# Performance work log

Hardware: AMD Instinct MI355X
Metric: run time of the kernel (lower is better)

Reference implementation:

```python
import jax, jax.numpy as jnp
import numpy as np


def _overlap_add_fft_conv(signal, kernel):
    """Vectorized overlap-add FFT convolution.

    signal: (B, K, T) float; kernel: (B, K, R) float.
    Returns (B, K, T), identical math to the torch per-block loop (the
    ortho-normed rfft/irfft pair on the signal cancels, kernel rfft uses
    default backward norm, exactly as in the original code).
    """
    B, K, T = signal.shape
    R = kernel.shape[-1]
    fft_len = 2 << (R - 1).bit_length()          # e.g. R=4000 -> 8192
    step = fft_len - R + 1                        # hop between blocks
    pad_len = (-T) % step                         # pad T up to multiple of step
    L = T + pad_len
    n_blocks = L // step

    # split padded signal into non-overlapping blocks, zero-pad each to fft_len
    sig = jnp.pad(signal, ((0, 0), (0, 0), (0, pad_len)))
    blocks = sig.reshape(B, K, n_blocks, step)
    blocks = jnp.pad(blocks, ((0, 0), (0, 0), (0, 0), (0, fft_len - step)))

    kernel_fft = jnp.fft.rfft(
        jnp.pad(kernel, ((0, 0), (0, 0), (0, fft_len - R))))      # (B,K,F)
    block_fft = jnp.fft.rfft(blocks, norm='ortho')                # (B,K,n_blocks,F)
    conv = jnp.fft.irfft(block_fft * kernel_fft[:, :, None, :],
                         norm='ortho')                            # (B,K,n_blocks,fft_len)

    # overlap-add: block i contributes at offset i*step, length fft_len
    idx = jnp.arange(n_blocks)[:, None] * step + jnp.arange(fft_len)[None, :]
    out = jnp.zeros((B, K, L + R - 1), dtype=conv.dtype)
    out = out.at[:, :, idx].add(conv)
    return out[:, :, :T]


def setup_inputs() -> dict:
    key = jax.random.key(0)
    k1, k2 = jax.random.split(key)
    onsets = jax.random.normal(k1, (8, 8, 262144), dtype=jnp.float32)
    sources = jax.random.normal(k2, (8, 8, 4000), dtype=jnp.float32)
    return {"onsets": onsets, "sources": sources, "delay_compensation": 0}


def reference(onsets, sources, delay_compensation):
    # delay_compensation is unused in the original module as well
    return _overlap_add_fft_conv(onsets, sources)
```

## Files before the change

kernel.cpp:

```cpp
#include <hip/hip_runtime.h>

#define T_LEN 262144
#define R_LEN 4000
#define NCH 64
#define WIN 12288
#define NCHUNK 126
#define V_OFF 4032

typedef __attribute__((ext_vector_type(8))) short bf16x8;
typedef __attribute__((ext_vector_type(4))) float f32x4;

static __device__ __forceinline__ unsigned short f2bf(float f) {
  unsigned u = __builtin_bit_cast(unsigned, f);
  unsigned r = 0x7FFFu + ((u >> 16) & 1u);
  return (unsigned short)((u + r) >> 16);
}

__global__ __launch_bounds__(256) void build_btf(const float* __restrict__ src,
                                                 unsigned short* __restrict__ btf) {
  int t = blockIdx.x * blockDim.x + threadIdx.x;
  if (t >= NCH * NCHUNK * 64) return;
  int lane = t & 63;
  int pm1 = (t >> 6) % NCHUNK;
  int ch = t / (64 * NCHUNK);
  int p = pm1 + 1;
  int j = lane & 15;
  int vbase = 32 * p + 8 * (lane >> 4);
  const float* k = src + (size_t)ch * R_LEN;
  unsigned short vals[8];
#pragma unroll
  for (int e = 0; e < 8; ++e) {
    int r = V_OFF + j - (vbase + e);
    float f = (r >= 0 && r < R_LEN) ? k[r] : 0.0f;
    vals[e] = f2bf(f);
  }
  unsigned int o0 = (unsigned int)vals[0] | ((unsigned int)vals[1] << 16);
  unsigned int o1 = (unsigned int)vals[2] | ((unsigned int)vals[3] << 16);
  unsigned int o2 = (unsigned int)vals[4] | ((unsigned int)vals[5] << 16);
  unsigned int o3 = (unsigned int)vals[6] | ((unsigned int)vals[7] << 16);
  unsigned int* dst = (unsigned int*)(btf + (size_t)t * 8);
  dst[0] = o0; dst[1] = o1; dst[2] = o2; dst[3] = o3;
}

__global__ __launch_bounds__(256) void conv_main(const float* __restrict__ x,
                                                 const unsigned short* __restrict__ btf,
                                                 float* __restrict__ out) {
  __shared__ unsigned short xs[WIN];
  const int bid = blockIdx.x;
  const int ch = bid >> 5;
  const int T0 = (bid & 31) << 13;
  const float* xch = x + (size_t)ch * T_LEN;

  const int base = T0 - V_OFF;
  for (int u = threadIdx.x * 4; u < WIN; u += 1024) {
    int gi = base + u;
    float4 v;
    if (gi >= 0 && gi <= T_LEN - 4) {
      v = *(const float4*)(xch + gi);
    } else {
      v.x = (gi     >= 0 && gi     < T_LEN) ? xch[gi]     : 0.f;
      v.y = (gi + 1 >= 0 && gi + 1 < T_LEN) ? xch[gi + 1] : 0.f;
      v.z = (gi + 2 >= 0 && gi + 2 < T_LEN) ? xch[gi + 2] : 0.f;
      v.w = (gi + 3 >= 0 && gi + 3 < T_LEN) ? xch[gi + 3] : 0.f;
    }
    unsigned long long pk = (unsigned long long)f2bf(v.x)
                          | ((unsigned long long)f2bf(v.y) << 16)
                          | ((unsigned long long)f2bf(v.z) << 32)
                          | ((unsigned long long)f2bf(v.w) << 48);
    *(unsigned long long*)(xs + u) = pk;
  }
  __syncthreads();

  const int lane = threadIdx.x & 63;
  const int w = threadIdx.x >> 6;
  const int i16 = lane & 15;
  const int g = lane >> 4;

  f32x4 acc[8] = {};
  const bf16x8* bp = (const bf16x8*)btf + (size_t)ch * NCHUNK * 64 + lane;
  const int abase = w * 2048 + 16 * i16 + 8 * g;

  for (int p = 1; p <= NCHUNK; ++p) {
    bf16x8 bfrag = bp[(size_t)(p - 1) * 64];
    const unsigned short* ap = xs + abase + 32 * p;
#pragma unroll
    for (int m = 0; m < 8; ++m) {
      bf16x8 afrag = *(const bf16x8*)(ap + m * 256);
      acc[m] = __builtin_amdgcn_mfma_f32_16x16x32_bf16(afrag, bfrag, acc[m], 0, 0, 0);
    }
  }

  float* och = out + (size_t)ch * T_LEN + T0 + w * 2048;
#pragma unroll
  for (int m = 0; m < 8; ++m) {
    int tb = m * 256 + i16;
#pragma unroll
    for (int r = 0; r < 4; ++r) {
      och[tb + 16 * (4 * g + r)] = acc[m][r];
    }
  }
}

extern "C" void kernel_launch(void* const* d_in, const int* in_sizes, int n_in,
                              void* d_out, int out_size, void* d_ws, size_t ws_size,
                              hipStream_t stream) {
  const float* onsets  = (const float*)d_in[0];
  const float* sources = (const float*)d_in[1];
  unsigned short* btf  = (unsigned short*)d_ws;
  float* out = (float*)d_out;

  int nthr = NCH * NCHUNK * 64;
  build_btf<<<(nthr + 255) / 256, 256, 0, stream>>>(sources, btf);
  conv_main<<<NCH * 32, 256, 0, stream>>>(onsets, btf, out);
}
```

Before: 125.1 us.

## Switch direct convolution to 32x32x16 MFMA with larger per-block tiles

```diff
diff --git a/kernel.cpp b/kernel.cpp
--- a/kernel.cpp
+++ b/kernel.cpp
@@ -3,12 +3,12 @@
 #define T_LEN 262144
 #define R_LEN 4000
 #define NCH 64
-#define WIN 12288
-#define NCHUNK 126
 #define V_OFF 4032
+#define NCHUNK 252
+#define WIN 36864
 
 typedef __attribute__((ext_vector_type(8))) short bf16x8;
-typedef __attribute__((ext_vector_type(4))) float f32x4;
+typedef __attribute__((ext_vector_type(16))) float f32x16;
 
 static __device__ __forceinline__ unsigned short f2bf(float f) {
   unsigned u = __builtin_bit_cast(unsigned, f);
@@ -18,85 +18,96 @@
 
 __global__ __launch_bounds__(256) void build_btf(const float* __restrict__ src,
                                                  unsigned short* __restrict__ btf) {
-  int t = blockIdx.x * blockDim.x + threadIdx.x;
+  int t = blockIdx.x * 256 + threadIdx.x;
   if (t >= NCH * NCHUNK * 64) return;
   int lane = t & 63;
-  int pm1 = (t >> 6) % NCHUNK;
+  int p = (t >> 6) % NCHUNK;
   int ch = t / (64 * NCHUNK);
-  int p = pm1 + 1;
-  int j = lane & 15;
-  int vbase = 32 * p + 8 * (lane >> 4);
+  int j = lane & 31;
+  int h = lane >> 5;
+  int kbase = 4000 + j - 16 * p - 8 * h;
   const float* k = src + (size_t)ch * R_LEN;
   unsigned short vals[8];
 #pragma unroll
   for (int e = 0; e < 8; ++e) {
-    int r = V_OFF + j - (vbase + e);
+    int r = kbase - e;
     float f = (r >= 0 && r < R_LEN) ? k[r] : 0.0f;
     vals[e] = f2bf(f);
   }
-  unsigned int o0 = (unsigned int)vals[0] | ((unsigned int)vals[1] << 16);
-  unsigned int o1 = (unsigned int)vals[2] | ((unsigned int)vals[3] << 16);
-  unsigned int o2 = (unsigned int)vals[4] | ((unsigned int)vals[5] << 16);
-  unsigned int o3 = (unsigned int)vals[6] | ((unsigned int)vals[7] << 16);
   unsigned int* dst = (unsigned int*)(btf + (size_t)t * 8);
-  dst[0] = o0; dst[1] = o1; dst[2] = o2; dst[3] = o3;
+  dst[0] = (unsigned int)vals[0] | ((unsigned int)vals[1] << 16);
+  dst[1] = (unsigned int)vals[2] | ((unsigned int)vals[3] << 16);
+  dst[2] = (unsigned int)vals[4] | ((unsigned int)vals[5] << 16);
+  dst[3] = (unsigned int)vals[6] | ((unsigned int)vals[7] << 16);
 }
 
-__global__ __launch_bounds__(256) void conv_main(const float* __restrict__ x,
-                                                 const unsigned short* __restrict__ btf,
-                                                 float* __restrict__ out) {
+__global__ __launch_bounds__(256, 2) void conv_main(const float* __restrict__ x,
+                                                    const unsigned short* __restrict__ btf,
+                                                    float* __restrict__ out) {
   __shared__ unsigned short xs[WIN];
   const int bid = blockIdx.x;
-  const int ch = bid >> 5;
-  const int T0 = (bid & 31) << 13;
+  const int ch = bid & 63;
+  const int T0 = (bid >> 6) << 15;
   const float* xch = x + (size_t)ch * T_LEN;
 
-  const int base = T0 - V_OFF;
-  for (int u = threadIdx.x * 4; u < WIN; u += 1024) {
-    int gi = base + u;
-    float4 v;
-    if (gi >= 0 && gi <= T_LEN - 4) {
-      v = *(const float4*)(xch + gi);
+  for (int s = threadIdx.x; s < WIN / 8; s += 256) {
+    int gi = T0 - 4000 + 8 * s;
+    float v0, v1, v2, v3, v4, v5, v6, v7;
+    if (gi >= 0 && gi + 8 <= T_LEN) {
+      float4 a = *(const float4*)(xch + gi);
+      float4 b = *(const float4*)(xch + gi + 4);
+      v0 = a.x; v1 = a.y; v2 = a.z; v3 = a.w;
+      v4 = b.x; v5 = b.y; v6 = b.z; v7 = b.w;
     } else {
-      v.x = (gi     >= 0 && gi     < T_LEN) ? xch[gi]     : 0.f;
-      v.y = (gi + 1 >= 0 && gi + 1 < T_LEN) ? xch[gi + 1] : 0.f;
-      v.z = (gi + 2 >= 0 && gi + 2 < T_LEN) ? xch[gi + 2] : 0.f;
-      v.w = (gi + 3 >= 0 && gi + 3 < T_LEN) ? xch[gi + 3] : 0.f;
+      v0 = (gi + 0 >= 0 && gi + 0 < T_LEN) ? xch[gi + 0] : 0.f;
+      v1 = (gi + 1 >= 0 && gi + 1 < T_LEN) ? xch[gi + 1] : 0.f;
+      v2 = (gi + 2 >= 0 && gi + 2 < T_LEN) ? xch[gi + 2] : 0.f;
+      v3 = (gi + 3 >= 0 && gi + 3 < T_LEN) ? xch[gi + 3] : 0.f;
+      v4 = (gi + 4 >= 0 && gi + 4 < T_LEN) ? xch[gi + 4] : 0.f;
+      v5 = (gi + 5 >= 0 && gi + 5 < T_LEN) ? xch[gi + 5] : 0.f;
+      v6 = (gi + 6 >= 0 && gi + 6 < T_LEN) ? xch[gi + 6] : 0.f;
+      v7 = (gi + 7 >= 0 && gi + 7 < T_LEN) ? xch[gi + 7] : 0.f;
     }
-    unsigned long long pk = (unsigned long long)f2bf(v.x)
-                          | ((unsigned long long)f2bf(v.y) << 16)
-                          | ((unsigned long long)f2bf(v.z) << 32)
-                          | ((unsigned long long)f2bf(v.w) << 48);
-    *(unsigned long long*)(xs + u) = pk;
+    uint4 pk;
+    pk.x = (unsigned int)f2bf(v0) | ((unsigned int)f2bf(v1) << 16);
+    pk.y = (unsigned int)f2bf(v2) | ((unsigned int)f2bf(v3) << 16);
+    pk.z = (unsigned int)f2bf(v4) | ((unsigned int)f2bf(v5) << 16);
+    pk.w = (unsigned int)f2bf(v6) | ((unsigned int)f2bf(v7) << 16);
+    int b = 16 * s;
+    b ^= ((b >> 7) & 1) << 5;
+    *(uint4*)((char*)xs + b) = pk;
   }
   __syncthreads();
 
   const int lane = threadIdx.x & 63;
   const int w = threadIdx.x >> 6;
-  const int i16 = lane & 15;
-  const int g = lane >> 4;
+  const int i = lane & 31;
+  const int h = lane >> 5;
 
-  f32x4 acc[8] = {};
+  f32x16 acc[8] = {};
+
   const bf16x8* bp = (const bf16x8*)btf + (size_t)ch * NCHUNK * 64 + lane;
-  const int abase = w * 2048 + 16 * i16 + 8 * g;
+  const int abase = 16384 * w + 64 * i + 16 * h;
 
-  for (int p = 1; p <= NCHUNK; ++p) {
-    bf16x8 bfrag = bp[(size_t)(p - 1) * 64];
-    const unsigned short* ap = xs + abase + 32 * p;
+#pragma unroll 2
+  for (int p = 0; p < NCHUNK; ++p) {
+    bf16x8 bfrag = bp[p * 64];
 #pragma unroll
     for (int m = 0; m < 8; ++m) {
-      bf16x8 afrag = *(const bf16x8*)(ap + m * 256);
-      acc[m] = __builtin_amdgcn_mfma_f32_16x16x32_bf16(afrag, bfrag, acc[m], 0, 0, 0);
+      int b = abase + 32 * p + 2048 * m;
+      b ^= ((b >> 7) & 1) << 5;
+      bf16x8 afrag = *(const bf16x8*)((const char*)xs + b);
+      acc[m] = __builtin_amdgcn_mfma_f32_32x32x16_bf16(afrag, bfrag, acc[m], 0, 0, 0);
     }
   }
 
-  float* och = out + (size_t)ch * T_LEN + T0 + w * 2048;
+  float* och = out + (size_t)ch * T_LEN + T0 + 8192 * w;
 #pragma unroll
   for (int m = 0; m < 8; ++m) {
-    int tb = m * 256 + i16;
 #pragma unroll
-    for (int r = 0; r < 4; ++r) {
-      och[tb + 16 * (4 * g + r)] = acc[m][r];
+    for (int r = 0; r < 16; ++r) {
+      int row = (r & 3) + 8 * (r >> 2) + 4 * h;
+      och[1024 * m + 32 * row + i] = acc[m][r];
     }
   }
 }
@@ -111,5 +122,5 @@
 
   int nthr = NCH * NCHUNK * 64;
   build_btf<<<(nthr + 255) / 256, 256, 0, stream>>>(sources, btf);
-  conv_main<<<NCH * 32, 256, 0, stream>>>(onsets, btf, out);
+  conv_main<<<512, 256, 0, stream>>>(onsets, btf, out);
 }
```

Result: slower. 148.1 us (+18.3%).
